# Optimization experiments

Measured on AMD Instinct MI355X. Metric: run time of the kernel, lower is better.

## Reference

```python
import jax, jax.numpy as jnp
from jax import lax
import numpy as np

V, D, H, CO = 50000, 300, 512, 100
B, S, W = 64, 32, 128


def setup_inputs() -> dict:
    key = jax.random.key(0)
    ks = jax.random.split(key, 24)
    sc = 0.1  # mimic uniform(-0.1, 0.1)-style small init; keeps tanh unsaturated
    inp = {
        "paragraphs": jax.random.randint(ks[0], (B, S, W), 0, V, dtype=jnp.int64),
        "embed_table": jax.random.normal(ks[1], (V, D), jnp.float32),
        "conv_w3": jax.random.normal(ks[2], (CO, 1, 3, D), jnp.float32) * 0.05,
        "conv_b3": jax.random.normal(ks[3], (CO,), jnp.float32) * sc,
        "conv_w4": jax.random.normal(ks[4], (CO, 1, 4, D), jnp.float32) * 0.05,
        "conv_b4": jax.random.normal(ks[5], (CO,), jnp.float32) * sc,
        "conv_w5": jax.random.normal(ks[6], (CO, 1, 5, D), jnp.float32) * 0.05,
        "conv_b5": jax.random.normal(ks[7], (CO,), jnp.float32) * sc,
        "proj_w": jax.random.normal(ks[8], (300, 300), jnp.float32) * sc,
        "proj_b": jax.random.normal(ks[9], (300,), jnp.float32) * sc,
        "init_w": jax.random.normal(ks[10], (H, 300), jnp.float32) * sc,
        "init_b": jax.random.normal(ks[11], (H,), jnp.float32) * sc,
        "w_ih_f": jax.random.normal(ks[12], (H, 300), jnp.float32) * sc,
        "w_hh_f": jax.random.normal(ks[13], (H, H), jnp.float32) * sc,
        "b_ih_f": jax.random.normal(ks[14], (H,), jnp.float32) * sc,
        "b_hh_f": jax.random.normal(ks[15], (H,), jnp.float32) * sc,
        "w_ih_b": jax.random.normal(ks[16], (H, 300), jnp.float32) * sc,
        "w_hh_b": jax.random.normal(ks[17], (H, H), jnp.float32) * sc,
        "b_ih_b": jax.random.normal(ks[18], (H,), jnp.float32) * sc,
        "b_hh_b": jax.random.normal(ks[19], (H,), jnp.float32) * sc,
        "cls_w": jax.random.normal(ks[20], (5, 2 * H), jnp.float32) * sc,
        "cls_b": jax.random.normal(ks[21], (5,), jnp.float32) * sc,
    }
    return inp


def _cnn_text(tok, embed_table, conv_params):
    # tok: (N, W) int ids -> (N, 3*CO) sentence features (dropout = eval identity)
    emb = embed_table[tok]              # (N, W, D)
    x = emb[:, None, :, :]              # (N, 1, W, D)
    feats = []
    for w, b in conv_params:
        y = lax.conv_general_dilated(
            x, w, window_strides=(1, 1), padding="VALID",
            dimension_numbers=("NCHW", "OIHW", "NCHW"))  # (N, CO, W-K+1, 1)
        y = jax.nn.relu(y[..., 0] + b[None, :, None])       # (N, CO, W-K+1)
        feats.append(jnp.max(y, axis=2))                    # (N, CO) max-pool over time
    return jnp.concatenate(feats, axis=1)                    # (N, 3*CO)


def reference(paragraphs, embed_table, conv_w3, conv_b3, conv_w4, conv_b4,
              conv_w5, conv_b5, proj_w, proj_b, init_w, init_b,
              w_ih_f, w_hh_f, b_ih_f, b_hh_f, w_ih_b, w_hh_b, b_ih_b, b_hh_b,
              cls_w, cls_b):
    b_, s_, w_ = paragraphs.shape
    tok = paragraphs.reshape(b_ * s_, w_)
    conv_params = [(conv_w3, conv_b3), (conv_w4, conv_b4), (conv_w5, conv_b5)]
    sent = _cnn_text(tok, embed_table, conv_params).reshape(b_, s_, 3 * CO)

    # init_rnn: same init hidden for both directions
    h0 = sent[:, 0, :] @ init_w.T + init_b  # (B, H)

    def step(carry, x_t):
        hf, hb = carry
        xi = x_t @ proj_w.T + proj_b  # (B, 300)
        hf_n = jnp.tanh(xi @ w_ih_f.T + b_ih_f + hf @ w_hh_f.T + b_hh_f)
        hb_n = jnp.tanh(xi @ w_ih_b.T + b_ih_b + hb @ w_hh_b.T + b_hh_b)
        pred = jnp.concatenate([hf_n, hb_n], axis=1) @ cls_w.T + cls_b  # (B, 5)
        return (hf_n, hb_n), pred

    _, preds = lax.scan(step, (h0, h0), jnp.swapaxes(sent, 0, 1))  # (S, B, 5)
    return jnp.swapaxes(preds, 0, 1)  # (B, S, 5)
```

## Files before the change

### kernel.cpp

```cpp
#include <hip/hip_runtime.h>


#define LDSK     304
#define LDSROWB  608
#define LDSBYTES 80256

typedef __bf16   bf16x8 __attribute__((ext_vector_type(8)));
typedef float    f32x16 __attribute__((ext_vector_type(16)));
typedef _Float16 h2v    __attribute__((ext_vector_type(2)));

#define MFMA32(a, b, c) __builtin_amdgcn_mfma_f32_32x32x16_bf16((a), (b), (c), 0, 0, 0)

__device__ __forceinline__ unsigned int packf16(float a, float b) {
  h2v h; h[0] = (_Float16)a; h[1] = (_Float16)b;
  return __builtin_bit_cast(unsigned int, h);
}

__global__ void prep_all(const float* __restrict__ e, __bf16* __restrict__ eh,
                         const float* __restrict__ w3, const float* __restrict__ w4,
                         const float* __restrict__ w5, __bf16* __restrict__ Aw32,
                         const float* __restrict__ whf, const float* __restrict__ whb,
                         uint4* __restrict__ Wq) {
  const int bid = blockIdx.x;
  if (bid < 7325) {
    long i = ((long)bid * 256 + threadIdx.x) * 8;
    if (i >= 15000000L) return;
    float4 a = *(const float4*)(e + i);
    float4 b = *(const float4*)(e + i + 4);
    union { __bf16 h[8]; uint4 u; } pk;
    pk.h[0] = (__bf16)a.x; pk.h[1] = (__bf16)a.y; pk.h[2] = (__bf16)a.z; pk.h[3] = (__bf16)a.w;
    pk.h[4] = (__bf16)b.x; pk.h[5] = (__bf16)b.y; pk.h[6] = (__bf16)b.z; pk.h[7] = (__bf16)b.w;
    *(uint4*)(eh + i) = pk.u;
  } else if (bid < 9149) {
    int idx = (bid - 7325) * 256 + threadIdx.x;
    if (idx >= 48 * 19 * 64 * 8) return;
    int i    = idx & 7;
    int lane = (idx >> 3) & 63;
    int rem  = idx >> 9;
    int ks   = rem % 19, g = rem / 19;
    int kc, cg, j; const float* w;
    if (g < 12)      { kc = 3; cg = g / 3;        j = g % 3;        w = w3; }
    else if (g < 28) { kc = 4; cg = (g - 12) / 4; j = (g - 12) % 4; w = w4; }
    else             { kc = 5; cg = (g - 28) / 5; j = (g - 28) % 5; w = w5; }
    int ch = cg * 32 + (lane & 31);
    int k  = ks * 16 + (lane >> 5) * 8 + i;
    float v = 0.f;
    if (ch < 100 && k < 300) v = w[(ch * kc + j) * 300 + k];
    Aw32[idx] = (__bf16)v;
  } else {
    int idx = (bid - 9149) * 256 + threadIdx.x;
    if (idx >= 2 * 128 * 256) return;
    int dir = idx >> 15;
    int rem = idx & 32767;
    int kq = rem >> 8, tid = rem & 255;
    const float* W = dir ? whb : whf;
    const float* r0 = W + (size_t)tid * 512 + 4 * kq;
    const float* r1 = W + (size_t)(tid + 256) * 512 + 4 * kq;
    uint4 o;
    o.x = packf16(r0[0], r0[1]);
    o.y = packf16(r1[0], r1[1]);
    o.z = packf16(r0[2], r0[3]);
    o.w = packf16(r1[2], r1[3]);
    Wq[idx] = o;
  }
}

__device__ __forceinline__ void conv_chunk1(const char* ldsc, const __bf16* __restrict__ Aw32,
                                            int GB, int kc, int cg,
                                            const float* __restrict__ bias,
                                            int colbase, int pmax,
                                            float* __restrict__ srow, int lane) {
  const int m32 = lane & 31, hi = lane >> 5;
  f32x16 acc[4];
#pragma unroll
  for (int n = 0; n < 4; ++n)
#pragma unroll
    for (int e = 0; e < 16; ++e) acc[n][e] = 0.f;

  for (int j = 0; j < kc; ++j) {
    const int row0 = m32 + j;
    const int mask = (row0 & 7) << 4;
    const int rowbyte = row0 * LDSROWB + hi * 16;
    const __bf16* a0 = Aw32 + (size_t)(GB + cg * kc + j) * (19 * 512) + lane * 8;
#pragma unroll 2
    for (int ks = 0; ks < 19; ++ks) {
      bf16x8 bf[4];
#pragma unroll
      for (int nt = 0; nt < 4; ++nt) {
        int addr = rowbyte + nt * (32 * LDSROWB) + ks * 32;
        bf[nt] = *(const bf16x8*)(ldsc + (addr ^ mask));
      }
      bf16x8 af = *(const bf16x8*)(a0 + ks * 512);
#pragma unroll
      for (int nt = 0; nt < 4; ++nt)
        acc[nt] = MFMA32(af, bf[nt], acc[nt]);
    }
  }
  float m[16];
#pragma unroll
  for (int r = 0; r < 16; ++r) m[r] = -3.0e38f;
#pragma unroll
  for (int nt = 0; nt < 4; ++nt) {
    int p = nt * 32 + m32;
    bool valid = (p <= pmax);
#pragma unroll
    for (int r = 0; r < 16; ++r)
      m[r] = fmaxf(m[r], valid ? acc[nt][r] : -3.0e38f);
  }
#pragma unroll
  for (int r = 0; r < 16; ++r) {
#pragma unroll
    for (int d = 1; d < 32; d <<= 1) m[r] = fmaxf(m[r], __shfl_xor(m[r], d, 64));
  }
  if (m32 == 0) {
#pragma unroll
    for (int r = 0; r < 16; ++r) {
      int ch = cg * 32 + (r & 3) + 8 * (r >> 2) + 4 * hi;
      if (ch < 100) srow[colbase + ch] = fmaxf(m[r] + bias[ch], 0.f);
    }
  }
}

__global__ void __launch_bounds__(512, 4)
conv_kernel(const int* __restrict__ tok, const __bf16* __restrict__ embh,
            const __bf16* __restrict__ Aw32,
            const float* __restrict__ b3, const float* __restrict__ b4, const float* __restrict__ b5,
            float* __restrict__ sent) {
  extern __shared__ __bf16 lds[];
  char* ldsc = (char*)lds;
  const int sid = blockIdx.x, tid = threadIdx.x;
  const int* t0 = tok + sid * 128;
  const char* eb = (const char*)embh;
  for (int i = tid; i < 4 * 76; i += 512) {
    int r = 128 + i / 76, q = i - (i / 76) * 76;
    *(uint2*)(ldsc + ((r * LDSROWB + q * 8) ^ ((r & 7) << 4))) = (uint2){0u, 0u};
  }
  if (tid < 128) {
    *(uint2*)(ldsc + ((tid * LDSROWB + 600) ^ ((tid & 7) << 4))) = (uint2){0u, 0u};
  }
  for (int i = tid; i < 128 * 75; i += 512) {
    int r = i / 75, q = i - r * 75;
    long tk = (long)t0[r];
    uint2 v = *(const uint2*)(eb + tk * 600L + q * 8);
    *(uint2*)(ldsc + ((r * LDSROWB + q * 8) ^ ((r & 7) << 4))) = v;
  }
  __syncthreads();
  const int wave = tid >> 6, lane = tid & 63;
  float* srow = sent + (size_t)sid * 304;
  if (wave < 4) {
    conv_chunk1(ldsc, Aw32, 28, 5, wave, b5, 200, 123, srow, lane);
    conv_chunk1(ldsc, Aw32,  0, 3, wave, b3,   0, 125, srow, lane);
  } else {
    conv_chunk1(ldsc, Aw32, 12, 4, wave - 4, b4, 100, 124, srow, lane);
  }
}

__global__ void xigh0_kernel(const float* __restrict__ sent,
                             const float* __restrict__ pw, const float* __restrict__ pb,
                             const float* __restrict__ wf, const float* __restrict__ wb,
                             const float* __restrict__ bif, const float* __restrict__ bhf,
                             const float* __restrict__ bib, const float* __restrict__ bhb,
                             const float* __restrict__ iw, const float* __restrict__ ib,
                             float* __restrict__ G, float* __restrict__ h0) {
  __shared__ float s[4][300];
  __shared__ float xi[4][304];
  const int tid = threadIdx.x;
  if (blockIdx.x < 512) {
    const int rb = blockIdx.x * 4;
    for (int i = tid; i < 4 * 300; i += 256) {
      int r = i / 300, c = i - r * 300;
      s[r][c] = sent[(size_t)(rb + r) * 304 + c];
    }
    __syncthreads();
    for (int o = tid; o < 300; o += 256) {
      const float* w = pw + o * 300;
      float bvv = pb[o];
      float a[4];
#pragma unroll
      for (int r = 0; r < 4; ++r) a[r] = bvv;
      for (int k = 0; k < 300; k += 4) {
        float4 wv = *(const float4*)(w + k);
#pragma unroll
        for (int r = 0; r < 4; ++r)
          a[r] += wv.x * s[r][k] + wv.y * s[r][k + 1] + wv.z * s[r][k + 2] + wv.w * s[r][k + 3];
      }
#pragma unroll
      for (int r = 0; r < 4; ++r) xi[r][o] = a[r];
    }
    __syncthreads();
    for (int o = tid; o < 1024; o += 256) {
      int dir = o >> 9, oo = o & 511;
      const float* w = (dir ? wb : wf) + oo * 300;
      float bvv = dir ? (bib[oo] + bhb[oo]) : (bif[oo] + bhf[oo]);
      float a[4];
#pragma unroll
      for (int r = 0; r < 4; ++r) a[r] = bvv;
      for (int k = 0; k < 300; k += 4) {
        float4 wv = *(const float4*)(w + k);
#pragma unroll
        for (int r = 0; r < 4; ++r)
          a[r] += wv.x * xi[r][k] + wv.y * xi[r][k + 1] + wv.z * xi[r][k + 2] + wv.w * xi[r][k + 3];
      }
#pragma unroll
      for (int r = 0; r < 4; ++r) G[(rb + r) * 1024 + o] = a[r];
    }
  } else {
    const int bb = (blockIdx.x - 512) * 4;
    for (int i = tid; i < 4 * 300; i += 256) {
      int r = i / 300, c = i - r * 300;
      s[r][c] = sent[(size_t)((bb + r) * 32) * 304 + c];
    }
    __syncthreads();
    for (int o = tid; o < 512; o += 256) {
      const float* w = iw + o * 300;
      float bvv = ib[o];
      float a[4];
#pragma unroll
      for (int r = 0; r < 4; ++r) a[r] = bvv;
      for (int k = 0; k < 300; k += 4) {
        float4 wv = *(const float4*)(w + k);
#pragma unroll
        for (int r = 0; r < 4; ++r)
          a[r] += wv.x * s[r][k] + wv.y * s[r][k + 1] + wv.z * s[r][k + 2] + wv.w * s[r][k + 3];
      }
#pragma unroll
      for (int r = 0; r < 4; ++r) h0[(bb + r) * 512 + o] = a[r];
    }
  }
}

#if __has_builtin(__builtin_amdgcn_fdot2)
#define FDOT2(a, b, c) __builtin_amdgcn_fdot2((a), (b), (c), false)
#else
static __device__ __forceinline__ float FDOT2(h2v a, h2v b, float c) {
  return c + (float)a[0] * (float)b[0] + (float)a[1] * (float)b[1];
}
#endif
__device__ __forceinline__ h2v as_h2(unsigned int u) { return __builtin_bit_cast(h2v, u); }

__global__ void __launch_bounds__(1024)
rnn_kernel(const uint4* __restrict__ Wq, const float* __restrict__ G,
           const float* __restrict__ h0, float* __restrict__ H) {
  const int blk = blockIdx.x, tid = threadIdx.x;
  const int dir = blk >> 5, b0 = (blk & 31) * 2;
  const int o = tid & 255, kh = (tid >> 8) & 3;
  __shared__ float hs[2][512];
  __shared__ uint2 h2p[2][128];
  __shared__ float part[4][2][512];
  {
    int c = tid >> 9, oo = tid & 511;
    hs[c][oo] = h0[(b0 + c) * 512 + oo];
  }
  __syncthreads();
  const uint4* W = Wq + (size_t)dir * (128 * 256);
  for (int t = 0; t < 32; ++t) {
    if (tid < 256) {
      int c = tid >> 7, kq = tid & 127;
      h2p[c][kq] = (uint2){packf16(hs[c][4 * kq], hs[c][4 * kq + 1]),
                           packf16(hs[c][4 * kq + 2], hs[c][4 * kq + 3])};
    }
    __syncthreads();
    float a00 = 0.f, a01 = 0.f, a10 = 0.f, a11 = 0.f;
    const int kb = kh * 32;
#pragma unroll 4
    for (int kk = 0; kk < 32; ++kk) {
      int kq = kb + kk;
      uint4 w = W[kq * 256 + o];
      uint2 p0 = h2p[0][kq], p1 = h2p[1][kq];
      a00 = FDOT2(as_h2(w.x), as_h2(p0.x), a00); a00 = FDOT2(as_h2(w.z), as_h2(p0.y), a00);
      a01 = FDOT2(as_h2(w.y), as_h2(p0.x), a01); a01 = FDOT2(as_h2(w.w), as_h2(p0.y), a01);
      a10 = FDOT2(as_h2(w.x), as_h2(p1.x), a10); a10 = FDOT2(as_h2(w.z), as_h2(p1.y), a10);
      a11 = FDOT2(as_h2(w.y), as_h2(p1.x), a11); a11 = FDOT2(as_h2(w.w), as_h2(p1.y), a11);
    }
    part[kh][0][o] = a00; part[kh][0][o + 256] = a01;
    part[kh][1][o] = a10; part[kh][1][o + 256] = a11;
    __syncthreads();
    {
      int c = tid >> 9, oo = tid & 511;
      const float* g = G + (size_t)((b0 + c) * 32 + t) * 1024 + dir * 512;
      float s = g[oo] + ((part[0][c][oo] + part[1][c][oo]) + (part[2][c][oo] + part[3][c][oo]));
      float n = tanhf(s);
      hs[c][oo] = n;
      H[(size_t)((dir * 64 + b0 + c) * 32 + t) * 512 + oo] = n;
    }
    __syncthreads();
  }
}

__global__ void pred_kernel(const float* __restrict__ H, const float* __restrict__ cw,
                            const float* __restrict__ cb, float* __restrict__ out) {
  const int bt = blockIdx.x * 4 + (threadIdx.x >> 6);
  const int lane = threadIdx.x & 63;
  const int b = bt >> 5, t = bt & 31;
  const float* hf = H + ((size_t)(b * 32 + t)) * 512;
  const float* hb = H + ((size_t)((64 + b) * 32 + t)) * 512;
  for (int c = 0; c < 5; ++c) {
    const float* w = cw + c * 1024;
    float a = 0.f;
    for (int o = lane; o < 512; o += 64) a += w[o] * hf[o] + w[512 + o] * hb[o];
#pragma unroll
    for (int d = 32; d; d >>= 1) a += __shfl_down(a, d, 64);
    if (lane == 0) out[bt * 5 + c] = a + cb[c];
  }
}

extern "C" void kernel_launch(void* const* d_in, const int* in_sizes, int n_in,
                              void* d_out, int out_size, void* d_ws, size_t ws_size,
                              hipStream_t stream) {
  const int*   tok  = (const int*)d_in[0];
  const float* emb  = (const float*)d_in[1];
  const float* w3   = (const float*)d_in[2];
  const float* b3   = (const float*)d_in[3];
  const float* w4   = (const float*)d_in[4];
  const float* b4   = (const float*)d_in[5];
  const float* w5   = (const float*)d_in[6];
  const float* b5   = (const float*)d_in[7];
  const float* pw   = (const float*)d_in[8];
  const float* pb   = (const float*)d_in[9];
  const float* iw   = (const float*)d_in[10];
  const float* ib   = (const float*)d_in[11];
  const float* wihf = (const float*)d_in[12];
  const float* whhf = (const float*)d_in[13];
  const float* bihf = (const float*)d_in[14];
  const float* bhhf = (const float*)d_in[15];
  const float* wihb = (const float*)d_in[16];
  const float* whhb = (const float*)d_in[17];
  const float* bihb = (const float*)d_in[18];
  const float* bhhb = (const float*)d_in[19];
  const float* cw   = (const float*)d_in[20];
  const float* cb   = (const float*)d_in[21];
  float* out = (float*)d_out;

  char* ws = (char*)d_ws;
  __bf16* Aw32  = (__bf16*)(ws);
  uint4* Wq     = (uint4*)(ws +  1u * 1024 * 1024);
  float* sent   = (float*)(ws +  2u * 1024 * 1024);
  __bf16* embh  = (__bf16*)(ws + 8u * 1024 * 1024);
  float* G      = (float*)(ws +  8u * 1024 * 1024);
  float* h0     = (float*)(ws + 16u * 1024 * 1024);
  float* H      = (float*)(ws + 17u * 1024 * 1024);

  prep_all<<<9405, 256, 0, stream>>>(emb, embh, w3, w4, w5, Aw32, whhf, whhb, Wq);

  hipFuncSetAttribute(reinterpret_cast<const void*>(conv_kernel),
                      hipFuncAttributeMaxDynamicSharedMemorySize, LDSBYTES);
  conv_kernel<<<2048, 512, LDSBYTES, stream>>>(tok, embh, Aw32, b3, b4, b5, sent);

  xigh0_kernel<<<528, 256, 0, stream>>>(sent, pw, pb, wihf, wihb, bihf, bhhf, bihb, bhhb,
                                        iw, ib, G, h0);
  rnn_kernel<<<64, 1024, 0, stream>>>(Wq, G, h0, H);
  pred_kernel<<<512, 256, 0, stream>>>(H, cw, cb, out);
}
```

Measured before the change: 527.9 us.

## Use packed fp16 k-major weights in xi/G kernel and fuse classifier into RNN

Pre-packs the projection and input-to-hidden weights into k-major fp16 pairs during prep, so the xi/G kernel reads coalesced weights and uses fdot2 instead of strided fp32 row loads. The RNN kernel now computes each direction's classifier partial sums per timestep from shared memory, which removes the full hidden-state write to global memory and the separate pred kernel. A tiny final kernel adds the two directions and the bias. This lowers precision to fp16 for these GEMMs and adds a reduction to every step of the serial RNN loop.

```diff
diff --git a/kernel.cpp b/kernel.cpp
--- a/kernel.cpp
+++ b/kernel.cpp
@@ -15,12 +15,23 @@
   h2v h; h[0] = (_Float16)a; h[1] = (_Float16)b;
   return __builtin_bit_cast(unsigned int, h);
 }
+#if __has_builtin(__builtin_amdgcn_fdot2)
+#define FDOT2(a, b, c) __builtin_amdgcn_fdot2((a), (b), (c), false)
+#else
+static __device__ __forceinline__ float FDOT2(h2v a, h2v b, float c) {
+  return c + (float)a[0] * (float)b[0] + (float)a[1] * (float)b[1];
+}
+#endif
+__device__ __forceinline__ h2v as_h2(unsigned int u) { return __builtin_bit_cast(h2v, u); }
 
 __global__ void prep_all(const float* __restrict__ e, __bf16* __restrict__ eh,
                          const float* __restrict__ w3, const float* __restrict__ w4,
                          const float* __restrict__ w5, __bf16* __restrict__ Aw32,
                          const float* __restrict__ whf, const float* __restrict__ whb,
-                         uint4* __restrict__ Wq) {
+                         uint4* __restrict__ Wq,
+                         const float* __restrict__ pw, unsigned int* __restrict__ pwh2,
+                         const float* __restrict__ wf, const float* __restrict__ wb,
+                         unsigned int* __restrict__ wih2) {
   const int bid = blockIdx.x;
   if (bid < 7325) {
     long i = ((long)bid * 256 + threadIdx.x) * 8;
@@ -47,7 +58,7 @@
     float v = 0.f;
     if (ch < 100 && k < 300) v = w[(ch * kc + j) * 300 + k];
     Aw32[idx] = (__bf16)v;
-  } else {
+  } else if (bid < 9405) {
     int idx = (bid - 9149) * 256 + threadIdx.x;
     if (idx >= 2 * 128 * 256) return;
     int dir = idx >> 15;
@@ -62,6 +73,17 @@
     o.z = packf16(r0[2], r0[3]);
     o.w = packf16(r1[2], r1[3]);
     Wq[idx] = o;
+  } else if (bid < 9581) {
+    int idx = (bid - 9405) * 256 + threadIdx.x;
+    if (idx >= 150 * 300) return;
+    int kp = idx / 300, o = idx - kp * 300;
+    pwh2[idx] = packf16(pw[o * 300 + 2 * kp], pw[o * 300 + 2 * kp + 1]);
+  } else {
+    int idx = (bid - 9581) * 256 + threadIdx.x;
+    if (idx >= 150 * 1024) return;
+    int kp = idx >> 10, o = idx & 1023;
+    const float* w = (o < 512) ? (wf + (size_t)o * 300) : (wb + (size_t)(o - 512) * 300);
+    wih2[idx] = packf16(w[2 * kp], w[2 * kp + 1]);
   }
 }
 
@@ -156,59 +178,69 @@
 }
 
 __global__ void xigh0_kernel(const float* __restrict__ sent,
-                             const float* __restrict__ pw, const float* __restrict__ pb,
-                             const float* __restrict__ wf, const float* __restrict__ wb,
+                             const unsigned int* __restrict__ pwh2, const float* __restrict__ pb,
+                             const unsigned int* __restrict__ wih2,
                              const float* __restrict__ bif, const float* __restrict__ bhf,
                              const float* __restrict__ bib, const float* __restrict__ bhb,
                              const float* __restrict__ iw, const float* __restrict__ ib,
                              float* __restrict__ G, float* __restrict__ h0) {
-  __shared__ float s[4][300];
-  __shared__ float xi[4][304];
+  __shared__ float xif[4][304];
+  __shared__ uint4 s2k[150];
+  __shared__ uint4 xi2k[150];
   const int tid = threadIdx.x;
   if (blockIdx.x < 512) {
     const int rb = blockIdx.x * 4;
-    for (int i = tid; i < 4 * 300; i += 256) {
-      int r = i / 300, c = i - r * 300;
-      s[r][c] = sent[(size_t)(rb + r) * 304 + c];
+    for (int i = tid; i < 600; i += 256) {
+      int kp = i >> 2, r = i & 3;
+      float2 v = *(const float2*)(sent + (size_t)(rb + r) * 304 + 2 * kp);
+      ((unsigned int*)s2k)[kp * 4 + r] = packf16(v.x, v.y);
     }
     __syncthreads();
     for (int o = tid; o < 300; o += 256) {
-      const float* w = pw + o * 300;
-      float bvv = pb[o];
       float a[4];
 #pragma unroll
-      for (int r = 0; r < 4; ++r) a[r] = bvv;
-      for (int k = 0; k < 300; k += 4) {
-        float4 wv = *(const float4*)(w + k);
-#pragma unroll
-        for (int r = 0; r < 4; ++r)
-          a[r] += wv.x * s[r][k] + wv.y * s[r][k + 1] + wv.z * s[r][k + 2] + wv.w * s[r][k + 3];
+      for (int r = 0; r < 4; ++r) a[r] = pb[o];
+#pragma unroll 2
+      for (int kp = 0; kp < 150; ++kp) {
+        h2v w = as_h2(pwh2[kp * 300 + o]);
+        uint4 sv = s2k[kp];
+        a[0] = FDOT2(w, as_h2(sv.x), a[0]);
+        a[1] = FDOT2(w, as_h2(sv.y), a[1]);
+        a[2] = FDOT2(w, as_h2(sv.z), a[2]);
+        a[3] = FDOT2(w, as_h2(sv.w), a[3]);
       }
 #pragma unroll
-      for (int r = 0; r < 4; ++r) xi[r][o] = a[r];
+      for (int r = 0; r < 4; ++r) xif[r][o] = a[r];
+    }
+    __syncthreads();
+    for (int i = tid; i < 600; i += 256) {
+      int kp = i >> 2, r = i & 3;
+      ((unsigned int*)xi2k)[kp * 4 + r] = packf16(xif[r][2 * kp], xif[r][2 * kp + 1]);
     }
     __syncthreads();
     for (int o = tid; o < 1024; o += 256) {
       int dir = o >> 9, oo = o & 511;
-      const float* w = (dir ? wb : wf) + oo * 300;
       float bvv = dir ? (bib[oo] + bhb[oo]) : (bif[oo] + bhf[oo]);
       float a[4];
 #pragma unroll
       for (int r = 0; r < 4; ++r) a[r] = bvv;
-      for (int k = 0; k < 300; k += 4) {
-        float4 wv = *(const float4*)(w + k);
-#pragma unroll
-        for (int r = 0; r < 4; ++r)
-          a[r] += wv.x * xi[r][k] + wv.y * xi[r][k + 1] + wv.z * xi[r][k + 2] + wv.w * xi[r][k + 3];
+#pragma unroll 2
+      for (int kp = 0; kp < 150; ++kp) {
+        h2v w = as_h2(wih2[kp * 1024 + o]);
+        uint4 xv = xi2k[kp];
+        a[0] = FDOT2(w, as_h2(xv.x), a[0]);
+        a[1] = FDOT2(w, as_h2(xv.y), a[1]);
+        a[2] = FDOT2(w, as_h2(xv.z), a[2]);
+        a[3] = FDOT2(w, as_h2(xv.w), a[3]);
       }
 #pragma unroll
-      for (int r = 0; r < 4; ++r) G[(rb + r) * 1024 + o] = a[r];
+      for (int r = 0; r < 4; ++r) G[(size_t)(rb + r) * 1024 + o] = a[r];
     }
   } else {
     const int bb = (blockIdx.x - 512) * 4;
     for (int i = tid; i < 4 * 300; i += 256) {
       int r = i / 300, c = i - r * 300;
-      s[r][c] = sent[(size_t)((bb + r) * 32) * 304 + c];
+      xif[r][c] = sent[(size_t)((bb + r) * 32) * 304 + c];
     }
     __syncthreads();
     for (int o = tid; o < 512; o += 256) {
@@ -221,26 +253,18 @@
         float4 wv = *(const float4*)(w + k);
 #pragma unroll
         for (int r = 0; r < 4; ++r)
-          a[r] += wv.x * s[r][k] + wv.y * s[r][k + 1] + wv.z * s[r][k + 2] + wv.w * s[r][k + 3];
+          a[r] += wv.x * xif[r][k] + wv.y * xif[r][k + 1] + wv.z * xif[r][k + 2] + wv.w * xif[r][k + 3];
       }
 #pragma unroll
       for (int r = 0; r < 4; ++r) h0[(bb + r) * 512 + o] = a[r];
     }
   }
 }
-
-#if __has_builtin(__builtin_amdgcn_fdot2)
-#define FDOT2(a, b, c) __builtin_amdgcn_fdot2((a), (b), (c), false)
-#else
-static __device__ __forceinline__ float FDOT2(h2v a, h2v b, float c) {
-  return c + (float)a[0] * (float)b[0] + (float)a[1] * (float)b[1];
-}
-#endif
-__device__ __forceinline__ h2v as_h2(unsigned int u) { return __builtin_bit_cast(h2v, u); }
 
 __global__ void __launch_bounds__(1024)
 rnn_kernel(const uint4* __restrict__ Wq, const float* __restrict__ G,
-           const float* __restrict__ h0, float* __restrict__ H) {
+           const float* __restrict__ h0, const float* __restrict__ cw,
+           float* __restrict__ PF, float* __restrict__ PB) {
   const int blk = blockIdx.x, tid = threadIdx.x;
   const int dir = blk >> 5, b0 = (blk & 31) * 2;
   const int o = tid & 255, kh = (tid >> 8) & 3;
@@ -251,6 +275,7 @@
     int c = tid >> 9, oo = tid & 511;
     hs[c][oo] = h0[(b0 + c) * 512 + oo];
   }
+  float* Pd = dir ? PB : PF;
   __syncthreads();
   const uint4* W = Wq + (size_t)dir * (128 * 256);
   for (int t = 0; t < 32; ++t) {
@@ -279,29 +304,27 @@
       int c = tid >> 9, oo = tid & 511;
       const float* g = G + (size_t)((b0 + c) * 32 + t) * 1024 + dir * 512;
       float s = g[oo] + ((part[0][c][oo] + part[1][c][oo]) + (part[2][c][oo] + part[3][c][oo]));
-      float n = tanhf(s);
-      hs[c][oo] = n;
-      H[(size_t)((dir * 64 + b0 + c) * 32 + t) * 512 + oo] = n;
-    }
-    __syncthreads();
-  }
-}
-
-__global__ void pred_kernel(const float* __restrict__ H, const float* __restrict__ cw,
-                            const float* __restrict__ cb, float* __restrict__ out) {
-  const int bt = blockIdx.x * 4 + (threadIdx.x >> 6);
-  const int lane = threadIdx.x & 63;
-  const int b = bt >> 5, t = bt & 31;
-  const float* hf = H + ((size_t)(b * 32 + t)) * 512;
-  const float* hb = H + ((size_t)((64 + b) * 32 + t)) * 512;
-  for (int c = 0; c < 5; ++c) {
-    const float* w = cw + c * 1024;
-    float a = 0.f;
-    for (int o = lane; o < 512; o += 64) a += w[o] * hf[o] + w[512 + o] * hb[o];
-#pragma unroll
-    for (int d = 32; d; d >>= 1) a += __shfl_down(a, d, 64);
-    if (lane == 0) out[bt * 5 + c] = a + cb[c];
-  }
+      hs[c][oo] = tanhf(s);
+    }
+    __syncthreads();
+    if (tid < 640) {
+      int ch = tid / 320, rem = tid - ch * 320;
+      int c5 = rem >> 6, ln = rem & 63;
+      const float* w = cw + c5 * 1024 + dir * 512;
+      float a = 0.f;
+#pragma unroll
+      for (int q = 0; q < 8; ++q) a += w[ln + q * 64] * hs[ch][ln + q * 64];
+#pragma unroll
+      for (int d = 32; d; d >>= 1) a += __shfl_down(a, d, 64);
+      if (ln == 0) Pd[((size_t)(b0 + ch) * 32 + t) * 5 + c5] = a;
+    }
+  }
+}
+
+__global__ void pred_final(const float* __restrict__ PF, const float* __restrict__ PB,
+                           const float* __restrict__ cb, float* __restrict__ out) {
+  int i = blockIdx.x * 256 + threadIdx.x;
+  if (i < 10240) out[i] = PF[i] + PB[i] + cb[i % 5];
 }
 
 extern "C" void kernel_launch(void* const* d_in, const int* in_sizes, int n_in,
@@ -335,19 +358,23 @@
   __bf16* Aw32  = (__bf16*)(ws);
   uint4* Wq     = (uint4*)(ws +  1u * 1024 * 1024);
   float* sent   = (float*)(ws +  2u * 1024 * 1024);
+  unsigned int* pwh2 = (unsigned int*)(ws + 4864u * 1024);
+  unsigned int* wih2 = (unsigned int*)(ws + 5120u * 1024);
+  float* PF     = (float*)(ws + 5888u * 1024);
+  float* PB     = (float*)(ws + 5988u * 1024);
   __bf16* embh  = (__bf16*)(ws + 8u * 1024 * 1024);
   float* G      = (float*)(ws +  8u * 1024 * 1024);
   float* h0     = (float*)(ws + 16u * 1024 * 1024);
-  float* H      = (float*)(ws + 17u * 1024 * 1024);
-
-  prep_all<<<9405, 256, 0, stream>>>(emb, embh, w3, w4, w5, Aw32, whhf, whhb, Wq);
+
+  prep_all<<<10181, 256, 0, stream>>>(emb, embh, w3, w4, w5, Aw32, whhf, whhb, Wq,
+                                      pw, pwh2, wihf, wihb, wih2);
 
   hipFuncSetAttribute(reinterpret_cast<const void*>(conv_kernel),
                       hipFuncAttributeMaxDynamicSharedMemorySize, LDSBYTES);
   conv_kernel<<<2048, 512, LDSBYTES, stream>>>(tok, embh, Aw32, b3, b4, b5, sent);
 
-  xigh0_kernel<<<528, 256, 0, stream>>>(sent, pw, pb, wihf, wihb, bihf, bhhf, bihb, bhhb,
+  xigh0_kernel<<<528, 256, 0, stream>>>(sent, pwh2, pb, wih2, bihf, bhhf, bihb, bhhb,
                                         iw, ib, G, h0);
-  rnn_kernel<<<64, 1024, 0, stream>>>(Wq, G, h0, H);
-  pred_kernel<<<512, 256, 0, stream>>>(H, cw, cb, out);
-}
+  rnn_kernel<<<64, 1024, 0, stream>>>(Wq, G, h0, cw, PF, PB);
+  pred_final<<<40, 256, 0, stream>>>(PF, PB, cb, out);
+}
```

Result: slower. 539.9 us (+2.3%).

## Split conv per sentence into two half-length blocks and merge maxima downstream

Applied to the files above, without the earlier changes.

Each sentence's convolution now runs as two blocks, each covering half of the 128 time positions plus a 4-row halo. The LDS footprint drops to about 41KB, and the accumulator count per wave halves. Each block writes partial max-pooled features, and the next kernel takes the elementwise max of the two halves while loading. The intent is higher occupancy and more parallelism in the conv stage. The cost is re-loading the halo rows, twice as many blocks, and doubled intermediate traffic.

```diff
diff --git a/kernel.cpp b/kernel.cpp
--- a/kernel.cpp
+++ b/kernel.cpp
@@ -3,7 +3,7 @@
 
 #define LDSK     304
 #define LDSROWB  608
-#define LDSBYTES 80256
+#define LDSBYTES 41344
 
 typedef __bf16   bf16x8 __attribute__((ext_vector_type(8)));
 typedef float    f32x16 __attribute__((ext_vector_type(16)));
@@ -68,12 +68,12 @@
 __device__ __forceinline__ void conv_chunk1(const char* ldsc, const __bf16* __restrict__ Aw32,
                                             int GB, int kc, int cg,
                                             const float* __restrict__ bias,
-                                            int colbase, int pmax,
-                                            float* __restrict__ srow, int lane) {
+                                            int colbase, int pmax, int pbase,
+                                            float* __restrict__ prow, int lane) {
   const int m32 = lane & 31, hi = lane >> 5;
-  f32x16 acc[4];
-#pragma unroll
-  for (int n = 0; n < 4; ++n)
+  f32x16 acc[2];
+#pragma unroll
+  for (int n = 0; n < 2; ++n)
 #pragma unroll
     for (int e = 0; e < 16; ++e) acc[n][e] = 0.f;
 
@@ -84,15 +84,15 @@
     const __bf16* a0 = Aw32 + (size_t)(GB + cg * kc + j) * (19 * 512) + lane * 8;
 #pragma unroll 2
     for (int ks = 0; ks < 19; ++ks) {
-      bf16x8 bf[4];
-#pragma unroll
-      for (int nt = 0; nt < 4; ++nt) {
+      bf16x8 bf[2];
+#pragma unroll
+      for (int nt = 0; nt < 2; ++nt) {
         int addr = rowbyte + nt * (32 * LDSROWB) + ks * 32;
         bf[nt] = *(const bf16x8*)(ldsc + (addr ^ mask));
       }
       bf16x8 af = *(const bf16x8*)(a0 + ks * 512);
 #pragma unroll
-      for (int nt = 0; nt < 4; ++nt)
+      for (int nt = 0; nt < 2; ++nt)
         acc[nt] = MFMA32(af, bf[nt], acc[nt]);
     }
   }
@@ -100,8 +100,8 @@
 #pragma unroll
   for (int r = 0; r < 16; ++r) m[r] = -3.0e38f;
 #pragma unroll
-  for (int nt = 0; nt < 4; ++nt) {
-    int p = nt * 32 + m32;
+  for (int nt = 0; nt < 2; ++nt) {
+    int p = pbase + nt * 32 + m32;
     bool valid = (p <= pmax);
 #pragma unroll
     for (int r = 0; r < 16; ++r)
@@ -116,29 +116,33 @@
 #pragma unroll
     for (int r = 0; r < 16; ++r) {
       int ch = cg * 32 + (r & 3) + 8 * (r >> 2) + 4 * hi;
-      if (ch < 100) srow[colbase + ch] = fmaxf(m[r] + bias[ch], 0.f);
-    }
-  }
-}
-
-__global__ void __launch_bounds__(512, 4)
+      if (ch < 100) prow[colbase + ch] = fmaxf(m[r] + bias[ch], 0.f);
+    }
+  }
+}
+
+__global__ void __launch_bounds__(512, 6)
 conv_kernel(const int* __restrict__ tok, const __bf16* __restrict__ embh,
             const __bf16* __restrict__ Aw32,
             const float* __restrict__ b3, const float* __restrict__ b4, const float* __restrict__ b5,
-            float* __restrict__ sent) {
+            float* __restrict__ sentP) {
   extern __shared__ __bf16 lds[];
   char* ldsc = (char*)lds;
-  const int sid = blockIdx.x, tid = threadIdx.x;
-  const int* t0 = tok + sid * 128;
+  const int bid = blockIdx.x, tid = threadIdx.x;
+  const int sid = bid >> 1, half = bid & 1;
+  const int* t0 = tok + sid * 128 + half * 64;
   const char* eb = (const char*)embh;
-  for (int i = tid; i < 4 * 76; i += 512) {
-    int r = 128 + i / 76, q = i - (i / 76) * 76;
-    *(uint2*)(ldsc + ((r * LDSROWB + q * 8) ^ ((r & 7) << 4))) = (uint2){0u, 0u};
-  }
-  if (tid < 128) {
+  const int nrows = half ? 64 : 68;
+  if (tid < 68) {
     *(uint2*)(ldsc + ((tid * LDSROWB + 600) ^ ((tid & 7) << 4))) = (uint2){0u, 0u};
   }
-  for (int i = tid; i < 128 * 75; i += 512) {
+  if (half) {
+    for (int i = tid; i < 4 * 75; i += 512) {
+      int r = 64 + i / 75, q = i - (i / 75) * 75;
+      *(uint2*)(ldsc + ((r * LDSROWB + q * 8) ^ ((r & 7) << 4))) = (uint2){0u, 0u};
+    }
+  }
+  for (int i = tid; i < nrows * 75; i += 512) {
     int r = i / 75, q = i - r * 75;
     long tk = (long)t0[r];
     uint2 v = *(const uint2*)(eb + tk * 600L + q * 8);
@@ -146,16 +150,17 @@
   }
   __syncthreads();
   const int wave = tid >> 6, lane = tid & 63;
-  float* srow = sent + (size_t)sid * 304;
+  const int pbase = half * 64;
+  float* prow = sentP + (size_t)(sid * 2 + half) * 304;
   if (wave < 4) {
-    conv_chunk1(ldsc, Aw32, 28, 5, wave, b5, 200, 123, srow, lane);
-    conv_chunk1(ldsc, Aw32,  0, 3, wave, b3,   0, 125, srow, lane);
+    conv_chunk1(ldsc, Aw32, 28, 5, wave, b5, 200, 123, pbase, prow, lane);
+    conv_chunk1(ldsc, Aw32,  0, 3, wave, b3,   0, 125, pbase, prow, lane);
   } else {
-    conv_chunk1(ldsc, Aw32, 12, 4, wave - 4, b4, 100, 124, srow, lane);
-  }
-}
-
-__global__ void xigh0_kernel(const float* __restrict__ sent,
+    conv_chunk1(ldsc, Aw32, 12, 4, wave - 4, b4, 100, 124, pbase, prow, lane);
+  }
+}
+
+__global__ void xigh0_kernel(const float* __restrict__ sentP,
                              const float* __restrict__ pw, const float* __restrict__ pb,
                              const float* __restrict__ wf, const float* __restrict__ wb,
                              const float* __restrict__ bif, const float* __restrict__ bhf,
@@ -169,7 +174,8 @@
     const int rb = blockIdx.x * 4;
     for (int i = tid; i < 4 * 300; i += 256) {
       int r = i / 300, c = i - r * 300;
-      s[r][c] = sent[(size_t)(rb + r) * 304 + c];
+      const float* p2 = sentP + (size_t)(rb + r) * 608;
+      s[r][c] = fmaxf(p2[c], p2[304 + c]);
     }
     __syncthreads();
     for (int o = tid; o < 300; o += 256) {
@@ -208,7 +214,8 @@
     const int bb = (blockIdx.x - 512) * 4;
     for (int i = tid; i < 4 * 300; i += 256) {
       int r = i / 300, c = i - r * 300;
-      s[r][c] = sent[(size_t)((bb + r) * 32) * 304 + c];
+      const float* p2 = sentP + (size_t)((bb + r) * 32) * 608;
+      s[r][c] = fmaxf(p2[c], p2[304 + c]);
     }
     __syncthreads();
     for (int o = tid; o < 512; o += 256) {
@@ -334,7 +341,7 @@
   char* ws = (char*)d_ws;
   __bf16* Aw32  = (__bf16*)(ws);
   uint4* Wq     = (uint4*)(ws +  1u * 1024 * 1024);
-  float* sent   = (float*)(ws +  2u * 1024 * 1024);
+  float* sentP  = (float*)(ws +  2u * 1024 * 1024);
   __bf16* embh  = (__bf16*)(ws + 8u * 1024 * 1024);
   float* G      = (float*)(ws +  8u * 1024 * 1024);
   float* h0     = (float*)(ws + 16u * 1024 * 1024);
@@ -342,11 +349,9 @@
 
   prep_all<<<9405, 256, 0, stream>>>(emb, embh, w3, w4, w5, Aw32, whhf, whhb, Wq);
 
-  hipFuncSetAttribute(reinterpret_cast<const void*>(conv_kernel),
-                      hipFuncAttributeMaxDynamicSharedMemorySize, LDSBYTES);
-  conv_kernel<<<2048, 512, LDSBYTES, stream>>>(tok, embh, Aw32, b3, b4, b5, sent);
-
-  xigh0_kernel<<<528, 256, 0, stream>>>(sent, pw, pb, wihf, wihb, bihf, bhhf, bihb, bhhb,
+  conv_kernel<<<4096, 512, LDSBYTES, stream>>>(tok, embh, Aw32, b3, b4, b5, sentP);
+
+  xigh0_kernel<<<528, 256, 0, stream>>>(sentP, pw, pb, wihf, wihb, bihf, bhhf, bihb, bhhb,
                                         iw, ib, G, h0);
   rnn_kernel<<<64, 1024, 0, stream>>>(Wq, G, h0, H);
   pred_kernel<<<512, 256, 0, stream>>>(H, cw, cb, out);
```

Result: slower. 558.0 us (+5.7%).
